# Kernel tuning notes

Hardware: AMD Instinct MI355X
Metric: run time of the kernel (lower is better)

The kernel has to match this reference:

```python
import jax, jax.numpy as jnp
import numpy as np

KERNEL_SIZE = 3
STRIDE = 1

def setup_inputs() -> dict:
    key = jax.random.key(0)
    kx, kw, kb = jax.random.split(key, 3)
    B, C_in, L = 32, 64, 16384
    C_out = 64
    x = jax.random.normal(kx, (B, C_in, L), dtype=jnp.float32)
    # original uses torch.rand (uniform [0,1)) for params
    weight = jax.random.uniform(kw, (C_out, C_in, KERNEL_SIZE), dtype=jnp.float32)
    bias = jax.random.uniform(kb, (C_out,), dtype=jnp.float32)
    return {"x": x, "weight": weight, "bias": bias}

def reference(x, weight, bias):
    # x: (B, C_in, L), weight: (C_out, C_in, K) -> out: (B, C_out, L_out)
    out = jax.lax.conv_general_dilated(
        x, weight,
        window_strides=(STRIDE,),
        padding="VALID",
        dimension_numbers=("NCH", "OIH", "NCH"),
    )
    return out + bias[None, :, None]
```

## Files before the change

kernel.cpp:

```cpp
#include <hip/hip_runtime.h>


typedef __bf16 bf16x8 __attribute__((ext_vector_type(8)));
typedef float f32x16 __attribute__((ext_vector_type(16)));
typedef float f32x4u __attribute__((ext_vector_type(4), aligned(4)));

#define C_IN 64
#define C_OUT 64
#define L_IN 16384
#define L_OUT 16382
#define NT 128
#define TILES 128
#define PW 200
#define XT_P 72
#define XT_COLS (NT + 4)

__global__ __launch_bounds__(256, 3) void conv1d_mfma(
    const float* __restrict__ x, const float* __restrict__ w,
    const float* __restrict__ bias, float* __restrict__ out) {
  __shared__ __align__(16) __bf16 wl[C_OUT * PW];
  __shared__ __align__(16) __bf16 xt[XT_COLS * XT_P];
  __shared__ float bias_s[C_OUT];

  const int t = threadIdx.x;
  const int bx = blockIdx.x;
  const int b = bx >> 7;
  const int tile = bx & 127;
  const int l0 = tile * NT;

  const float* xb = x + (size_t)b * (C_IN * L_IN);

  for (int i = t; i < C_OUT * 192; i += 256) {
    int co = i / 192;
    int r = i - co * 192;
    int ci = r / 3;
    int kk = r - ci * 3;
    wl[co * PW + kk * 64 + ci] = (__bf16)w[i];
  }
  if (t < C_OUT) bias_s[t] = bias[t];

  for (int idx = t; idx < C_IN * 33; idx += 256) {
    int ci = idx / 33;
    int cc = idx - ci * 33;
    int gc = l0 + cc * 4;
    if (gc > L_IN - 4) gc = L_IN - 4;
    f32x4u v = *(const f32x4u*)(xb + (size_t)ci * L_IN + gc);
    int col = cc * 4;
    xt[(col + 0) * XT_P + ci] = (__bf16)v[0];
    xt[(col + 1) * XT_P + ci] = (__bf16)v[1];
    xt[(col + 2) * XT_P + ci] = (__bf16)v[2];
    xt[(col + 3) * XT_P + ci] = (__bf16)v[3];
  }
  __syncthreads();

  const int lane = t & 63;
  const int wv = t >> 6;
  const int half = lane >> 5;
  const int ln = lane & 31;
  const int kh = half * 8;

  f32x16 acc0 = {}, acc1 = {};

#pragma unroll
  for (int s = 0; s < 12; ++s) {
    int kap = s * 16 + kh;
    int kk = kap >> 6;
    int ci0 = kap & 63;
    int col = wv * 32 + ln + kk;
    bf16x8 bf = *(const bf16x8*)&xt[col * XT_P + ci0];
    bf16x8 a0 = *(const bf16x8*)&wl[ln * PW + kap];
    bf16x8 a1 = *(const bf16x8*)&wl[(32 + ln) * PW + kap];
    acc0 = __builtin_amdgcn_mfma_f32_32x32x16_bf16(a0, bf, acc0, 0, 0, 0);
    acc1 = __builtin_amdgcn_mfma_f32_32x32x16_bf16(a1, bf, acc1, 0, 0, 0);
  }

  const int nl = wv * 32 + ln;
  const int ng = l0 + nl;
  if (tile != TILES - 1) {
#pragma unroll
    for (int h = 0; h < 2; ++h) {
#pragma unroll
      for (int r = 0; r < 16; ++r) {
        int co = h * 32 + 4 * half + (r & 3) + 8 * (r >> 2);
        float v = (h == 0 ? acc0[r] : acc1[r]) + bias_s[co];
        out[(size_t)(b * C_OUT + co) * L_OUT + ng] = v;
      }
    }
  } else {
#pragma unroll
    for (int h = 0; h < 2; ++h) {
#pragma unroll
      for (int r = 0; r < 16; ++r) {
        int co = h * 32 + 4 * half + (r & 3) + 8 * (r >> 2);
        float v = (h == 0 ? acc0[r] : acc1[r]) + bias_s[co];
        if (ng < L_OUT) out[(size_t)(b * C_OUT + co) * L_OUT + ng] = v;
      }
    }
  }
}

extern "C" void kernel_launch(void* const* d_in, const int* in_sizes, int n_in,
                              void* d_out, int out_size, void* d_ws, size_t ws_size,
                              hipStream_t stream) {
  const float* x = (const float*)d_in[0];
  const float* w = (const float*)d_in[1];
  const float* bias = (const float*)d_in[2];
  float* out = (float*)d_out;
  conv1d_mfma<<<dim3(32 * 128), dim3(256), 0, stream>>>(x, w, bias, out);
}
```

Baseline: 286.9 us.

## Make conv1d blocks persistent over eight sub-tiles with double-buffered LDS prefetch

Each block now covers eight consecutive 128-column sub-tiles instead of one. It keeps the weight fragments and bias in registers across them and double-buffers the transposed input tile in LDS, so the next tile's global loads overlap the current MFMAs. This spreads the per-block weight conversion and load over more output and hides load latency. In exchange the grid shrinks to 512 blocks with launch bounds of 2 blocks per SM, register pressure rises, and input loads become scalar loads instead of 4-wide vector loads.

```diff
diff --git a/kernel.cpp b/kernel.cpp
--- a/kernel.cpp
+++ b/kernel.cpp
@@ -3,31 +3,32 @@
 
 typedef __bf16 bf16x8 __attribute__((ext_vector_type(8)));
 typedef float f32x16 __attribute__((ext_vector_type(16)));
-typedef float f32x4u __attribute__((ext_vector_type(4), aligned(4)));
 
 #define C_IN 64
 #define C_OUT 64
 #define L_IN 16384
 #define L_OUT 16382
 #define NT 128
-#define TILES 128
+#define SUBT 8
+#define BT (NT * SUBT)
 #define PW 200
 #define XT_P 72
-#define XT_COLS (NT + 4)
+#define XT_COLS 132
+#define NLOAD 33
 
-__global__ __launch_bounds__(256, 3) void conv1d_mfma(
+__global__ __launch_bounds__(256, 2) void conv1d_mfma(
     const float* __restrict__ x, const float* __restrict__ w,
     const float* __restrict__ bias, float* __restrict__ out) {
   __shared__ __align__(16) __bf16 wl[C_OUT * PW];
-  __shared__ __align__(16) __bf16 xt[XT_COLS * XT_P];
+  __shared__ __align__(16) __bf16 xtA[XT_COLS * XT_P];
+  __shared__ __align__(16) __bf16 xtB[XT_COLS * XT_P];
   __shared__ float bias_s[C_OUT];
 
   const int t = threadIdx.x;
   const int bx = blockIdx.x;
-  const int b = bx >> 7;
-  const int tile = bx & 127;
-  const int l0 = tile * NT;
-
+  const int b = bx >> 4;
+  const int tile = bx & 15;
+  const int l0 = tile * BT;
   const float* xb = x + (size_t)b * (C_IN * L_IN);
 
   for (int i = t; i < C_OUT * 192; i += 256) {
@@ -39,64 +40,94 @@
   }
   if (t < C_OUT) bias_s[t] = bias[t];
 
-  for (int idx = t; idx < C_IN * 33; idx += 256) {
-    int ci = idx / 33;
-    int cc = idx - ci * 33;
-    int gc = l0 + cc * 4;
-    if (gc > L_IN - 4) gc = L_IN - 4;
-    f32x4u v = *(const f32x4u*)(xb + (size_t)ci * L_IN + gc);
-    int col = cc * 4;
-    xt[(col + 0) * XT_P + ci] = (__bf16)v[0];
-    xt[(col + 1) * XT_P + ci] = (__bf16)v[1];
-    xt[(col + 2) * XT_P + ci] = (__bf16)v[2];
-    xt[(col + 3) * XT_P + ci] = (__bf16)v[3];
-  }
-  __syncthreads();
-
   const int lane = t & 63;
   const int wv = t >> 6;
   const int half = lane >> 5;
   const int ln = lane & 31;
   const int kh = half * 8;
+  const int colbase = wv * 32 + ln;
 
-  f32x16 acc0 = {}, acc1 = {};
+#define STAGE_LOAD(BASE, SV)                                    \
+  _Pragma("unroll") for (int k = 0; k < NLOAD; ++k) {           \
+    int idx = t + k * 256;                                      \
+    int ci = idx / XT_COLS;                                     \
+    int col = idx - ci * XT_COLS;                               \
+    int gc = (BASE) + col;                                      \
+    gc = min(gc, L_IN - 1);   \
+    SV[k] = xb[(size_t)ci * L_IN + gc];                         \
+  }
 
+#define STAGE_WRITE(BUF, SV)                                    \
+  _Pragma("unroll") for (int k = 0; k < NLOAD; ++k) {           \
+    int idx = t + k * 256;                                      \
+    int ci = idx / XT_COLS;                                     \
+    int col = idx - ci * XT_COLS;                               \
+    BUF[col * XT_P + ci] = (__bf16)SV[k];                       \
+  }
+
+  {
+    float sv0[NLOAD];
+    STAGE_LOAD(l0, sv0)
+    STAGE_WRITE(xtA, sv0)
+  }
+  __syncthreads();
+
+  bf16x8 A0[12], A1[12];
 #pragma unroll
   for (int s = 0; s < 12; ++s) {
-    int kap = s * 16 + kh;
-    int kk = kap >> 6;
-    int ci0 = kap & 63;
-    int col = wv * 32 + ln + kk;
-    bf16x8 bf = *(const bf16x8*)&xt[col * XT_P + ci0];
-    bf16x8 a0 = *(const bf16x8*)&wl[ln * PW + kap];
-    bf16x8 a1 = *(const bf16x8*)&wl[(32 + ln) * PW + kap];
-    acc0 = __builtin_amdgcn_mfma_f32_32x32x16_bf16(a0, bf, acc0, 0, 0, 0);
-    acc1 = __builtin_amdgcn_mfma_f32_32x32x16_bf16(a1, bf, acc1, 0, 0, 0);
+    A0[s] = *(const bf16x8*)&wl[ln * PW + s * 16 + kh];
+    A1[s] = *(const bf16x8*)&wl[(32 + ln) * PW + s * 16 + kh];
+  }
+  float bs0[16], bs1[16];
+#pragma unroll
+  for (int r = 0; r < 16; ++r) {
+    int cl = 4 * half + (r & 3) + 8 * (r >> 2);
+    bs0[r] = bias_s[cl];
+    bs1[r] = bias_s[32 + cl];
   }
 
-  const int nl = wv * 32 + ln;
-  const int ng = l0 + nl;
-  if (tile != TILES - 1) {
-#pragma unroll
-    for (int h = 0; h < 2; ++h) {
-#pragma unroll
-      for (int r = 0; r < 16; ++r) {
-        int co = h * 32 + 4 * half + (r & 3) + 8 * (r >> 2);
-        float v = (h == 0 ? acc0[r] : acc1[r]) + bias_s[co];
-        out[(size_t)(b * C_OUT + co) * L_OUT + ng] = v;
-      }
-    }
-  } else {
-#pragma unroll
-    for (int h = 0; h < 2; ++h) {
-#pragma unroll
-      for (int r = 0; r < 16; ++r) {
-        int co = h * 32 + 4 * half + (r & 3) + 8 * (r >> 2);
-        float v = (h == 0 ? acc0[r] : acc1[r]) + bias_s[co];
-        if (ng < L_OUT) out[(size_t)(b * C_OUT + co) * L_OUT + ng] = v;
-      }
-    }
+#define PHASE(CUR, NXT, SS, ISLAST)                                          \
+  {                                                                          \
+    float sv[NLOAD];                                                         \
+    if (!(ISLAST)) { STAGE_LOAD(l0 + ((SS) + 1) * NT, sv) }                  \
+    f32x16 acc0, acc1;                                                       \
+    _Pragma("unroll") for (int r = 0; r < 16; ++r) {                         \
+      acc0[r] = bs0[r];                                                      \
+      acc1[r] = bs1[r];                                                      \
+    }                                                                        \
+    _Pragma("unroll") for (int s = 0; s < 12; ++s) {                         \
+      int kap = s * 16 + kh;                                                 \
+      int kk = kap >> 6;               \
+      int ci0 = kap & 63;                                                    \
+      bf16x8 bf = *(const bf16x8*)&CUR[(colbase + kk) * XT_P + ci0];         \
+      acc0 = __builtin_amdgcn_mfma_f32_32x32x16_bf16(A0[s], bf, acc0, 0, 0, 0); \
+      acc1 = __builtin_amdgcn_mfma_f32_32x32x16_bf16(A1[s], bf, acc1, 0, 0, 0); \
+    }                                                                        \
+    if (!(ISLAST)) { STAGE_WRITE(NXT, sv) }                                  \
+    {                                                                        \
+      int ng = l0 + (SS) * NT + colbase;                                     \
+      _Pragma("unroll") for (int r = 0; r < 16; ++r) {                       \
+        int cl = 4 * half + (r & 3) + 8 * (r >> 2);                          \
+        if ((SS) < SUBT - 1 || ng < L_OUT) {                                 \
+          out[(size_t)(b * C_OUT + cl) * L_OUT + ng] = acc0[r];              \
+          out[(size_t)(b * C_OUT + 32 + cl) * L_OUT + ng] = acc1[r];         \
+        }                                                                    \
+      }                                                                      \
+    }                                                                        \
+    __syncthreads();                                                         \
   }
+
+  PHASE(xtA, xtB, 0, 0)
+  PHASE(xtB, xtA, 1, 0)
+  PHASE(xtA, xtB, 2, 0)
+  PHASE(xtB, xtA, 3, 0)
+  PHASE(xtA, xtB, 4, 0)
+  PHASE(xtB, xtA, 5, 0)
+  PHASE(xtA, xtB, 6, 0)
+  PHASE(xtB, xtA, 7, 1)
+#undef PHASE
+#undef STAGE_LOAD
+#undef STAGE_WRITE
 }
 
 extern "C" void kernel_launch(void* const* d_in, const int* in_sizes, int n_in,
@@ -106,5 +137,5 @@
   const float* w = (const float*)d_in[1];
   const float* bias = (const float*)d_in[2];
   float* out = (float*)d_out;
-  conv1d_mfma<<<dim3(32 * 128), dim3(256), 0, stream>>>(x, w, bias, out);
+  conv1d_mfma<<<dim3(32 * 16), dim3(256), 0, stream>>>(x, w, bias, out);
 }
```

Result: slower. 412.1 us (+43.6%).

## Make blocks persistent over eight sub-tiles with register-prefetched input double buffering

Applied to the files above, without the earlier changes.

Each block now handles eight 64-column sub-tiles instead of one 128-column tile. This cuts the grid fourfold and amortises the per-block weight conversion into LDS across more output. While the current sub-tile is computed, the next input slice is prefetched into registers using scalar coalesced loads, then written to LDS between barriers. The work is also split across waves differently, one accumulator per wave over a 32x32 output quadrant, and launch bounds are raised for occupancy. The costs are only 1024 blocks (about four per CU), extra barriers per sub-tile, and scalar rather than vector global loads.

```diff
diff --git a/kernel.cpp b/kernel.cpp
--- a/kernel.cpp
+++ b/kernel.cpp
@@ -3,19 +3,20 @@
 
 typedef __bf16 bf16x8 __attribute__((ext_vector_type(8)));
 typedef float f32x16 __attribute__((ext_vector_type(16)));
-typedef float f32x4u __attribute__((ext_vector_type(4), aligned(4)));
 
 #define C_IN 64
 #define C_OUT 64
 #define L_IN 16384
 #define L_OUT 16382
-#define NT 128
-#define TILES 128
+#define NT 64
+#define SUBT 8
+#define BT (NT * SUBT)
 #define PW 200
 #define XT_P 72
-#define XT_COLS (NT + 4)
+#define XT_COLS 68
+#define NLOAD 17
 
-__global__ __launch_bounds__(256, 3) void conv1d_mfma(
+__global__ __launch_bounds__(256, 4) void conv1d_mfma(
     const float* __restrict__ x, const float* __restrict__ w,
     const float* __restrict__ bias, float* __restrict__ out) {
   __shared__ __align__(16) __bf16 wl[C_OUT * PW];
@@ -24,10 +25,9 @@
 
   const int t = threadIdx.x;
   const int bx = blockIdx.x;
-  const int b = bx >> 7;
-  const int tile = bx & 127;
-  const int l0 = tile * NT;
-
+  const int b = bx >> 5;
+  const int tile = bx & 31;
+  const int l0 = tile * BT;
   const float* xb = x + (size_t)b * (C_IN * L_IN);
 
   for (int i = t; i < C_OUT * 192; i += 256) {
@@ -39,62 +39,78 @@
   }
   if (t < C_OUT) bias_s[t] = bias[t];
 
-  for (int idx = t; idx < C_IN * 33; idx += 256) {
-    int ci = idx / 33;
-    int cc = idx - ci * 33;
-    int gc = l0 + cc * 4;
-    if (gc > L_IN - 4) gc = L_IN - 4;
-    f32x4u v = *(const f32x4u*)(xb + (size_t)ci * L_IN + gc);
-    int col = cc * 4;
-    xt[(col + 0) * XT_P + ci] = (__bf16)v[0];
-    xt[(col + 1) * XT_P + ci] = (__bf16)v[1];
-    xt[(col + 2) * XT_P + ci] = (__bf16)v[2];
-    xt[(col + 3) * XT_P + ci] = (__bf16)v[3];
-  }
-  __syncthreads();
-
   const int lane = t & 63;
   const int wv = t >> 6;
+  const int coh = wv >> 1;
+  const int colh = wv & 1;
   const int half = lane >> 5;
   const int ln = lane & 31;
   const int kh = half * 8;
 
-  f32x16 acc0 = {}, acc1 = {};
+  float sv[NLOAD];
+#pragma unroll
+  for (int k = 0; k < NLOAD; ++k) {
+    int idx = t + k * 256;
+    int ci = idx / XT_COLS;
+    int col = idx - ci * XT_COLS;
+    int gc = min(l0 + col, L_IN - 1);
+    sv[k] = xb[(size_t)ci * L_IN + gc];
+  }
+#pragma unroll
+  for (int k = 0; k < NLOAD; ++k) {
+    int idx = t + k * 256;
+    int ci = idx / XT_COLS;
+    int col = idx - ci * XT_COLS;
+    xt[col * XT_P + ci] = (__bf16)sv[k];
+  }
+  __syncthreads();
 
+  for (int ss = 0; ss < SUBT; ++ss) {
+    if (ss < SUBT - 1) {
 #pragma unroll
-  for (int s = 0; s < 12; ++s) {
-    int kap = s * 16 + kh;
-    int kk = kap >> 6;
-    int ci0 = kap & 63;
-    int col = wv * 32 + ln + kk;
-    bf16x8 bf = *(const bf16x8*)&xt[col * XT_P + ci0];
-    bf16x8 a0 = *(const bf16x8*)&wl[ln * PW + kap];
-    bf16x8 a1 = *(const bf16x8*)&wl[(32 + ln) * PW + kap];
-    acc0 = __builtin_amdgcn_mfma_f32_32x32x16_bf16(a0, bf, acc0, 0, 0, 0);
-    acc1 = __builtin_amdgcn_mfma_f32_32x32x16_bf16(a1, bf, acc1, 0, 0, 0);
-  }
-
-  const int nl = wv * 32 + ln;
-  const int ng = l0 + nl;
-  if (tile != TILES - 1) {
-#pragma unroll
-    for (int h = 0; h < 2; ++h) {
-#pragma unroll
-      for (int r = 0; r < 16; ++r) {
-        int co = h * 32 + 4 * half + (r & 3) + 8 * (r >> 2);
-        float v = (h == 0 ? acc0[r] : acc1[r]) + bias_s[co];
-        out[(size_t)(b * C_OUT + co) * L_OUT + ng] = v;
+      for (int k = 0; k < NLOAD; ++k) {
+        int idx = t + k * 256;
+        int ci = idx / XT_COLS;
+        int col = idx - ci * XT_COLS;
+        int gc = min(l0 + (ss + 1) * NT + col, L_IN - 1);
+        sv[k] = xb[(size_t)ci * L_IN + gc];
       }
     }
-  } else {
+
+    f32x16 acc = {};
 #pragma unroll
-    for (int h = 0; h < 2; ++h) {
+    for (int s = 0; s < 12; ++s) {
+      int kap = s * 16 + kh;
+      int kk = kap >> 6;
+      int ci0 = kap & 63;
+      bf16x8 av = *(const bf16x8*)&wl[(coh * 32 + ln) * PW + kap];
+      bf16x8 bv = *(const bf16x8*)&xt[(colh * 32 + ln + kk) * XT_P + ci0];
+      acc = __builtin_amdgcn_mfma_f32_32x32x16_bf16(av, bv, acc, 0, 0, 0);
+    }
+
+    {
+      int ng = l0 + ss * NT + colh * 32 + ln;
+      bool tail = (tile == 31 && ss == SUBT - 1);
+      if (!tail || ng < L_OUT) {
 #pragma unroll
-      for (int r = 0; r < 16; ++r) {
-        int co = h * 32 + 4 * half + (r & 3) + 8 * (r >> 2);
-        float v = (h == 0 ? acc0[r] : acc1[r]) + bias_s[co];
-        if (ng < L_OUT) out[(size_t)(b * C_OUT + co) * L_OUT + ng] = v;
+        for (int r = 0; r < 16; ++r) {
+          int cl = 4 * half + (r & 3) + 8 * (r >> 2);
+          int co = coh * 32 + cl;
+          out[(size_t)(b * C_OUT + co) * L_OUT + ng] = acc[r] + bias_s[co];
+        }
       }
+    }
+
+    __syncthreads();
+    if (ss < SUBT - 1) {
+#pragma unroll
+      for (int k = 0; k < NLOAD; ++k) {
+        int idx = t + k * 256;
+        int ci = idx / XT_COLS;
+        int col = idx - ci * XT_COLS;
+        xt[col * XT_P + ci] = (__bf16)sv[k];
+      }
+      __syncthreads();
     }
   }
 }
@@ -106,5 +122,5 @@
   const float* w = (const float*)d_in[1];
   const float* bias = (const float*)d_in[2];
   float* out = (float*)d_out;
-  conv1d_mfma<<<dim3(32 * 128), dim3(256), 0, stream>>>(x, w, bias, out);
+  conv1d_mfma<<<dim3(32 * 32), dim3(256), 0, stream>>>(x, w, bias, out);
 }
```

After: 283.5 us. About the same (-1.2%).
